# Performance work log

Measured on AMD Instinct MI355X. Metric: run time of the kernel, lower is better.

## Reference

```python
import jax, jax.numpy as jnp
import numpy as np

N = 200_000   # nodes
E = 6_400_000 # edges (avg degree 32)


def setup_inputs() -> dict:
    key = jax.random.key(0)
    k = jax.random.split(key, 6)
    x = jax.random.normal(k[0], (N, 2), dtype=jnp.float32)
    edge_index = jax.random.randint(k[1], (2, E), 0, N, dtype=jnp.int32)
    # GCNConv(2, 8) and GCNConv(8, 4) parameters (Glorot-ish init, zero bias as in PyG)
    W1 = jax.random.normal(k[2], (2, 8), dtype=jnp.float32) * (1.0 / np.sqrt(2.0))
    b1 = jnp.zeros((8,), dtype=jnp.float32)
    W2 = jax.random.normal(k[3], (8, 4), dtype=jnp.float32) * (1.0 / np.sqrt(8.0))
    b2 = jnp.zeros((4,), dtype=jnp.float32)
    return {"x": x, "edge_index": edge_index, "W1": W1, "b1": b1, "W2": W2, "b2": b2}


def _gcn_conv(x, src, dst, norm, W, b, n):
    # PyG GCNConv: linear transform, normalized gather/scatter-add, bias after aggregation
    h = x @ W                                   # [N, F_out]
    msg = h[src] * norm[:, None]                # gather + edge-wise scale, [E', F_out]
    agg = jax.ops.segment_sum(msg, dst, num_segments=n)  # scatter-add at targets
    return agg + b


def reference(x, edge_index, W1, b1, W2, b2):
    n = x.shape[0]
    # add self-loops (PyG default add_self_loops=True)
    loops = jnp.arange(n, dtype=edge_index.dtype)
    src = jnp.concatenate([edge_index[0], loops])
    dst = jnp.concatenate([edge_index[1], loops])
    # symmetric degree normalization: deg computed at targets with unit edge weights
    deg = jax.ops.segment_sum(jnp.ones_like(src, dtype=x.dtype), dst, num_segments=n)
    deg_inv_sqrt = jnp.where(deg > 0, jax.lax.rsqrt(jnp.maximum(deg, 1.0)), 0.0)
    norm = deg_inv_sqrt[src] * deg_inv_sqrt[dst]  # [E']

    h = jax.nn.relu(_gcn_conv(x, src, dst, norm, W1, b1, n))
    out = _gcn_conv(h, src, dst, norm, W2, b2, n)
    return out
```

## Files before the change

kernel.cpp:

```cpp
#include <hip/hip_runtime.h>


#define EPB   8192
#define PART  2048
#define LPBIT 11
#define SRCB  18
#define BC    4
#define RSTR  2049
#define STCAP 17408
#define NB    128


__global__ __launch_bounds__(512) void countA_kernel(
    const int* __restrict__ dst, int* __restrict__ cntmat, int E, int P) {
    __shared__ int cnt[128];
    int tid = threadIdx.x;
    if (tid < 128) cnt[tid] = 0;
    __syncthreads();
    int nv4 = E >> 2;
    int b4 = (blockIdx.x * EPB) >> 2;
    int e4 = min(b4 + (EPB >> 2), nv4);
    const int4* d4 = (const int4*)dst;
    #pragma unroll
    for (int k = 0; k < (EPB >> 2); k += 512) {
        int i = b4 + k + tid;
        if (i < e4) {
            int4 d = d4[i];
            atomicAdd(&cnt[d.x >> LPBIT], 1);
            atomicAdd(&cnt[d.y >> LPBIT], 1);
            atomicAdd(&cnt[d.z >> LPBIT], 1);
            atomicAdd(&cnt[d.w >> LPBIT], 1);
        }
    }
    if (blockIdx.x == gridDim.x - 1) {
        int e = (nv4 << 2) + tid;
        if (e < E) atomicAdd(&cnt[dst[e] >> LPBIT], 1);
    }
    __syncthreads();
    int* row = cntmat + (size_t)blockIdx.x * P;
    if (tid < P) row[tid] = cnt[tid];
}

__global__ __launch_bounds__(256) void colscanA_kernel(
    int* __restrict__ cntmat, int* __restrict__ colTotal, int B, int P) {
    __shared__ int sdata[256];
    int p = blockIdx.x, tid = threadIdx.x;
    int v[4];
    int s = 0;
    #pragma unroll
    for (int k = 0; k < 4; k++) {
        int b = tid * 4 + k;
        v[k] = (b < B) ? cntmat[(size_t)b * P + p] : 0;
        s += v[k];
    }
    int x = s;
    sdata[tid] = x;
    __syncthreads();
    for (int off = 1; off < 256; off <<= 1) {
        int t = (tid >= off) ? sdata[tid - off] : 0;
        __syncthreads();
        x += t;
        sdata[tid] = x;
        __syncthreads();
    }
    int run = x - s;
    #pragma unroll
    for (int k = 0; k < 4; k++) {
        int b = tid * 4 + k;
        if (b < B) cntmat[(size_t)b * P + p] = run;
        run += v[k];
    }
    if (tid == 255) colTotal[p] = x;
}

__global__ __launch_bounds__(256) void totalscanA_kernel(
    const int* __restrict__ colTotal, int* __restrict__ colStart,
    int P, int E) {
    __shared__ int sdata[256];
    int tid = threadIdx.x;
    int v[4];
    int s = 0;
    #pragma unroll
    for (int k = 0; k < 4; k++) {
        int i = tid * 4 + k;
        v[k] = (i < P) ? colTotal[i] : 0;
        s += v[k];
    }
    int x = s;
    sdata[tid] = x;
    __syncthreads();
    for (int off = 1; off < 256; off <<= 1) {
        int t = (tid >= off) ? sdata[tid - off] : 0;
        __syncthreads();
        x += t;
        sdata[tid] = x;
        __syncthreads();
    }
    int run = x - s;
    #pragma unroll
    for (int k = 0; k < 4; k++) {
        int i = tid * 4 + k;
        if (i < P) colStart[i] = run;
        run += v[k];
    }
    if (tid == 0) colStart[P] = E;
}

__global__ __launch_bounds__(512) void scatterA_kernel(
    const int* __restrict__ src, const int* __restrict__ dst,
    const int* __restrict__ cntmat, const int* __restrict__ colStart,
    unsigned* __restrict__ packed, int E, int P) {
    __shared__ int cur[128];
    int tid = threadIdx.x;
    if (tid < P) cur[tid] = colStart[tid] + cntmat[(size_t)blockIdx.x * P + tid];
    __syncthreads();
    int nv4 = E >> 2;
    int b4 = (blockIdx.x * EPB) >> 2;
    int e4 = min(b4 + (EPB >> 2), nv4);
    const int4* d4 = (const int4*)dst;
    const int4* s4 = (const int4*)src;
    #pragma unroll
    for (int k = 0; k < (EPB >> 2); k += 512) {
        int i = b4 + k + tid;
        if (i < e4) {
            int4 d = d4[i];
            int4 sv = s4[i];
            int p0 = atomicAdd(&cur[d.x >> LPBIT], 1);
            packed[p0] = ((unsigned)(d.x & (PART - 1)) << SRCB) | (unsigned)sv.x;
            int p1 = atomicAdd(&cur[d.y >> LPBIT], 1);
            packed[p1] = ((unsigned)(d.y & (PART - 1)) << SRCB) | (unsigned)sv.y;
            int p2 = atomicAdd(&cur[d.z >> LPBIT], 1);
            packed[p2] = ((unsigned)(d.z & (PART - 1)) << SRCB) | (unsigned)sv.z;
            int p3 = atomicAdd(&cur[d.w >> LPBIT], 1);
            packed[p3] = ((unsigned)(d.w & (PART - 1)) << SRCB) | (unsigned)sv.w;
        }
    }
    if (blockIdx.x == gridDim.x - 1) {
        int e = (nv4 << 2) + tid;
        if (e < E) {
            int d = dst[e];
            int pos = atomicAdd(&cur[d >> LPBIT], 1);
            packed[pos] = ((unsigned)(d & (PART - 1)) << SRCB) | (unsigned)src[e];
        }
    }
}


__global__ __launch_bounds__(512) void localC_kernel(
    const unsigned* __restrict__ packed, const int* __restrict__ colStart,
    int* __restrict__ runStart, int* __restrict__ sorted) {
    __shared__ int hist[PART];
    __shared__ int sdata[512];
    __shared__ unsigned stage[STCAP];
    int tid = threadIdx.x;
    int dp = blockIdx.x >> 2, b = blockIdx.x & (BC - 1);
    int s0 = colStart[dp], len = colStart[dp + 1] - s0;
    int lo = s0 + (int)(((long long)len * b) / BC);
    int hi = s0 + (int)(((long long)len * (b + 1)) / BC);
    for (int k = tid; k < PART; k += 512) hist[k] = 0;
    __syncthreads();
    for (int i = lo + tid; i < hi; i += 512)
        atomicAdd(&hist[packed[i] >> SRCB], 1);
    __syncthreads();
    int off = tid * 4;
    int v0 = hist[off], v1 = hist[off + 1], v2 = hist[off + 2], v3 = hist[off + 3];
    int s = v0 + v1 + v2 + v3;
    int x = s;
    sdata[tid] = x;
    __syncthreads();
    for (int o = 1; o < 512; o <<= 1) {
        int t = (tid >= o) ? sdata[tid - o] : 0;
        __syncthreads();
        x += t;
        sdata[tid] = x;
        __syncthreads();
    }
    int run = x - s;
    int* rs = runStart + (size_t)(dp * BC + b) * RSTR;
    int c0 = lo + run, c1 = c0 + v0, c2 = c1 + v1, c3 = c2 + v2;
    rs[off] = c0; rs[off + 1] = c1; rs[off + 2] = c2; rs[off + 3] = c3;
    __syncthreads();
    hist[off] = c0; hist[off + 1] = c1; hist[off + 2] = c2; hist[off + 3] = c3;
    if (tid == 0) rs[PART] = hi;
    __syncthreads();
    int total = hi - lo;
    bool ovf = total > STCAP;
    for (int i = lo + tid; i < hi; i += 512) {
        unsigned w = packed[i];
        int pos = atomicAdd(&hist[w >> SRCB], 1);
        if (!ovf) stage[pos - lo] = w;
        else sorted[pos] = (int)w;
    }
    __syncthreads();
    if (!ovf)
        for (int j = tid; j < total; j += 512) sorted[lo + j] = (int)stage[j];
}


__global__ __launch_bounds__(512) void dinvg_kernel(
    const int* __restrict__ runStart, const float* __restrict__ x,
    float* __restrict__ dinv, float* __restrict__ g, int n) {
    int i = blockIdx.x * 512 + threadIdx.x;
    if (i >= n) return;
    int dp = i >> LPBIT, ld = i & (PART - 1);
    int deg = 0;
    #pragma unroll
    for (int b = 0; b < BC; b++) {
        const int* rs = runStart + (size_t)(dp * BC + b) * RSTR + ld;
        deg += rs[1] - rs[0];
    }
    float d = rsqrtf((float)deg + 1.0f);
    dinv[i] = d;
    float2 xv = ((const float2*)x)[i];
    ((float2*)g)[i] = make_float2(xv.x * d, xv.y * d);
}


__global__ __launch_bounds__(512) void agg1f_kernel(
    const int* __restrict__ sorted, const int* __restrict__ runStart,
    const float* __restrict__ g, const float* __restrict__ dinv,
    const float* __restrict__ W1, const float* __restrict__ b1,
    const float* __restrict__ W2, float* __restrict__ hs2, int n) {
    __shared__ float acc[NB * 2];
    int tid = threadIdx.x;
    int i0 = blockIdx.x * NB;
    int dp = i0 >> LPBIT, l0 = i0 & (PART - 1);
    for (int k = tid; k < NB * 2; k += 512) acc[k] = 0.0f;
    __syncthreads();
    int lane = tid & 63;
    #pragma unroll
    for (int b = 0; b < BC; b++) {
        const int* rs = runStart + (size_t)(dp * BC + b) * RSTR;
        int lo = rs[l0], hi = rs[l0 + NB];
        for (int base = lo; base < hi; base += 512) {
            int e = base + tid;
            int sid = -1;
            float s0 = 0.0f, s1 = 0.0f;
            if (e < hi) {
                unsigned w = (unsigned)sorted[e];
                sid = (int)(w >> SRCB) - l0;
                int src = (int)(w & ((1u << SRCB) - 1));
                float2 gv = ((const float2*)g)[src];
                s0 = gv.x; s1 = gv.y;
            }
            #pragma unroll
            for (int off = 1; off < 64; off <<= 1) {
                int ps = __shfl_up(sid, off);
                float p0 = __shfl_up(s0, off);
                float p1 = __shfl_up(s1, off);
                if (lane >= off && ps == sid) { s0 += p0; s1 += p1; }
            }
            int ns = __shfl_down(sid, 1);
            bool tail = (lane == 63) || (ns != sid);
            if (tail && sid >= 0) {
                atomicAdd(&acc[sid * 2],     s0);
                atomicAdd(&acc[sid * 2 + 1], s1);
            }
        }
    }
    __syncthreads();
    if (tid < NB) {
        int i = i0 + tid;
        if (i < n) {
            float d = dinv[i];
            float2 gi = ((const float2*)g)[i];
            float s0 = (acc[tid * 2]     + gi.x) * d;
            float s1 = (acc[tid * 2 + 1] + gi.y) * d;
            float oc0 = 0.0f, oc1 = 0.0f, oc2 = 0.0f, oc3 = 0.0f;
            #pragma unroll
            for (int f = 0; f < 8; f++) {
                float h = fmaxf(s0 * W1[f] + s1 * W1[8 + f] + b1[f], 0.0f);
                oc0 += h * W2[4 * f];
                oc1 += h * W2[4 * f + 1];
                oc2 += h * W2[4 * f + 2];
                oc3 += h * W2[4 * f + 3];
            }
            float4 o;
            o.x = oc0 * d; o.y = oc1 * d; o.z = oc2 * d; o.w = oc3 * d;
            ((float4*)hs2)[i] = o;
        }
    }
}

__global__ __launch_bounds__(512) void agg2f_kernel(
    const int* __restrict__ sorted, const int* __restrict__ runStart,
    const float* __restrict__ hs2, const float* __restrict__ dinv,
    const float* __restrict__ b2, float* __restrict__ out, int n) {
    __shared__ float acc[NB * 4];
    int tid = threadIdx.x;
    int i0 = blockIdx.x * NB;
    int dp = i0 >> LPBIT, l0 = i0 & (PART - 1);
    for (int k = tid; k < NB * 4; k += 512) acc[k] = 0.0f;
    __syncthreads();
    int lane = tid & 63;
    #pragma unroll
    for (int b = 0; b < BC; b++) {
        const int* rs = runStart + (size_t)(dp * BC + b) * RSTR;
        int lo = rs[l0], hi = rs[l0 + NB];
        for (int base = lo; base < hi; base += 512) {
            int e = base + tid;
            int sid = -1;
            float s0 = 0.0f, s1 = 0.0f, s2 = 0.0f, s3 = 0.0f;
            if (e < hi) {
                unsigned w = (unsigned)sorted[e];
                sid = (int)(w >> SRCB) - l0;
                int src = (int)(w & ((1u << SRCB) - 1));
                float4 hv = ((const float4*)hs2)[src];
                s0 = hv.x; s1 = hv.y; s2 = hv.z; s3 = hv.w;
            }
            #pragma unroll
            for (int off = 1; off < 64; off <<= 1) {
                int ps = __shfl_up(sid, off);
                float p0 = __shfl_up(s0, off);
                float p1 = __shfl_up(s1, off);
                float p2 = __shfl_up(s2, off);
                float p3 = __shfl_up(s3, off);
                if (lane >= off && ps == sid) { s0 += p0; s1 += p1; s2 += p2; s3 += p3; }
            }
            int ns = __shfl_down(sid, 1);
            bool tail = (lane == 63) || (ns != sid);
            if (tail && sid >= 0) {
                atomicAdd(&acc[sid * 4],     s0);
                atomicAdd(&acc[sid * 4 + 1], s1);
                atomicAdd(&acc[sid * 4 + 2], s2);
                atomicAdd(&acc[sid * 4 + 3], s3);
            }
        }
    }
    __syncthreads();
    if (tid < NB) {
        int i = i0 + tid;
        if (i < n) {
            float d = dinv[i];
            float4 hv = ((const float4*)hs2)[i];
            float4 o;
            o.x = d * (acc[tid * 4]     + hv.x) + b2[0];
            o.y = d * (acc[tid * 4 + 1] + hv.y) + b2[1];
            o.z = d * (acc[tid * 4 + 2] + hv.z) + b2[2];
            o.w = d * (acc[tid * 4 + 3] + hv.w) + b2[3];
            ((float4*)out)[i] = o;
        }
    }
}

extern "C" void kernel_launch(void* const* d_in, const int* in_sizes, int n_in,
                              void* d_out, int out_size, void* d_ws, size_t ws_size,
                              hipStream_t stream) {
    const float* x   = (const float*)d_in[0];
    const int*   ei  = (const int*)d_in[1];
    const float* W1  = (const float*)d_in[2];
    const float* b1  = (const float*)d_in[3];
    const float* W2  = (const float*)d_in[4];
    const float* b2  = (const float*)d_in[5];
    float* out = (float*)d_out;

    const int n = in_sizes[0] / 2;
    const int E = in_sizes[1] / 2;
    const int* src = ei;
    const int* dst = ei + E;

    const int P  = (n + PART - 1) >> LPBIT;
    const int B1 = (E + EPB - 1) / EPB;

    int* ws = (int*)d_ws;
    int* colTotal = ws;
    int* colStart = ws + 1024;
    int* cntmatA  = ws + 2048;
    size_t cmsz = (((size_t)B1 * P) + 3) & ~(size_t)3;
    int* runStart = cntmatA + cmsz;
    size_t rssz = (((size_t)P * BC * RSTR) + 3) & ~(size_t)3;
    unsigned* packed = (unsigned*)(runStart + rssz);
    int* sorted = (int*)(packed + E);
    size_t nd = (size_t)P << LPBIT;
    float* dinv = (float*)packed;
    float* g    = dinv + nd;
    float* hs2  = g + 2 * nd;

    const int gN = (n + 511) / 512;
    const int gB = (n + NB - 1) / NB;

    countA_kernel    <<<B1, 512, 0, stream>>>(dst, cntmatA, E, P);
    colscanA_kernel  <<<P, 256, 0, stream>>>(cntmatA, colTotal, B1, P);
    totalscanA_kernel<<<1, 256, 0, stream>>>(colTotal, colStart, P, E);
    scatterA_kernel  <<<B1, 512, 0, stream>>>(src, dst, cntmatA, colStart, packed, E, P);
    localC_kernel    <<<P * BC, 512, 0, stream>>>(packed, colStart, runStart, sorted);
    dinvg_kernel     <<<gN, 512, 0, stream>>>(runStart, x, dinv, g, n);
    agg1f_kernel     <<<gB, 512, 0, stream>>>(sorted, runStart, g, dinv, W1, b1, W2, hs2, n);
    agg2f_kernel     <<<gB, 512, 0, stream>>>(sorted, runStart, hs2, dinv, b2, out, n);
}
```

Baseline: 272.1 us.

## Replace segmented wave-scan aggregation with LDS-staged gather and per-node reduction

```diff
diff --git a/kernel.cpp b/kernel.cpp
--- a/kernel.cpp
+++ b/kernel.cpp
@@ -9,6 +9,7 @@
 #define RSTR  2049
 #define STCAP 17408
 #define NB    128
+#define CAP   1536
 
 
 __global__ __launch_bounds__(512) void countA_kernel(
@@ -216,56 +217,61 @@
 }
 
 
-__global__ __launch_bounds__(512) void agg1f_kernel(
+__global__ __launch_bounds__(512) void agg1s_kernel(
     const int* __restrict__ sorted, const int* __restrict__ runStart,
     const float* __restrict__ g, const float* __restrict__ dinv,
     const float* __restrict__ W1, const float* __restrict__ b1,
     const float* __restrict__ W2, float* __restrict__ hs2, int n) {
-    __shared__ float acc[NB * 2];
+    __shared__ float2 stage2[CAP];
+    __shared__ int sb[BC][NB + 1];
+    __shared__ float sres[NB * 2];
+    float* stage = (float*)stage2;
     int tid = threadIdx.x;
     int i0 = blockIdx.x * NB;
     int dp = i0 >> LPBIT, l0 = i0 & (PART - 1);
-    for (int k = tid; k < NB * 2; k += 512) acc[k] = 0.0f;
-    __syncthreads();
-    int lane = tid & 63;
+    for (int k = tid; k < BC * (NB + 1); k += 512) {
+        int b = k / (NB + 1), idx = k - b * (NB + 1);
+        sb[b][idx] = runStart[(size_t)(dp * BC + b) * RSTR + l0 + idx];
+    }
+    int nid = tid >> 2;
+    int c = tid & 1;
+    int half = (tid >> 1) & 1;
+    float acc = 0.0f;
+    __syncthreads();
     #pragma unroll
     for (int b = 0; b < BC; b++) {
-        const int* rs = runStart + (size_t)(dp * BC + b) * RSTR;
-        int lo = rs[l0], hi = rs[l0 + NB];
-        for (int base = lo; base < hi; base += 512) {
-            int e = base + tid;
-            int sid = -1;
-            float s0 = 0.0f, s1 = 0.0f;
-            if (e < hi) {
+        int lo = sb[b][0], hi = sb[b][NB];
+        for (int e = lo + tid; e < hi; e += 512) {
+            int off = e - lo;
+            if (off < CAP) {
                 unsigned w = (unsigned)sorted[e];
-                sid = (int)(w >> SRCB) - l0;
                 int src = (int)(w & ((1u << SRCB) - 1));
-                float2 gv = ((const float2*)g)[src];
-                s0 = gv.x; s1 = gv.y;
-            }
-            #pragma unroll
-            for (int off = 1; off < 64; off <<= 1) {
-                int ps = __shfl_up(sid, off);
-                float p0 = __shfl_up(s0, off);
-                float p1 = __shfl_up(s1, off);
-                if (lane >= off && ps == sid) { s0 += p0; s1 += p1; }
-            }
-            int ns = __shfl_down(sid, 1);
-            bool tail = (lane == 63) || (ns != sid);
-            if (tail && sid >= 0) {
-                atomicAdd(&acc[sid * 2],     s0);
-                atomicAdd(&acc[sid * 2 + 1], s1);
-            }
-        }
-    }
+                stage2[off] = ((const float2*)g)[src];
+            }
+        }
+        __syncthreads();
+        int a = sb[b][nid] - lo, bnd = sb[b][nid + 1] - lo;
+        for (int j = a + half; j < bnd; j += 2) {
+            if (j < CAP) acc += stage[j * 2 + c];
+            else {
+                unsigned w = (unsigned)sorted[lo + j];
+                int src = (int)(w & ((1u << SRCB) - 1));
+                acc += g[2 * (size_t)src + c];
+            }
+        }
+        __syncthreads();
+    }
+    if (half == 1) sres[nid * 2 + c] = acc;
+    __syncthreads();
+    if (half == 0) sres[nid * 2 + c] += acc;
     __syncthreads();
     if (tid < NB) {
         int i = i0 + tid;
         if (i < n) {
             float d = dinv[i];
             float2 gi = ((const float2*)g)[i];
-            float s0 = (acc[tid * 2]     + gi.x) * d;
-            float s1 = (acc[tid * 2 + 1] + gi.y) * d;
+            float s0 = (sres[tid * 2] + gi.x) * d;
+            float s1 = (sres[tid * 2 + 1] + gi.y) * d;
             float oc0 = 0.0f, oc1 = 0.0f, oc2 = 0.0f, oc3 = 0.0f;
             #pragma unroll
             for (int f = 0; f < 8; f++) {
@@ -282,64 +288,51 @@
     }
 }
 
-__global__ __launch_bounds__(512) void agg2f_kernel(
+__global__ __launch_bounds__(512) void agg2s_kernel(
     const int* __restrict__ sorted, const int* __restrict__ runStart,
     const float* __restrict__ hs2, const float* __restrict__ dinv,
     const float* __restrict__ b2, float* __restrict__ out, int n) {
-    __shared__ float acc[NB * 4];
+    __shared__ float4 stage4[CAP];
+    __shared__ int sb[BC][NB + 1];
+    float* stage = (float*)stage4;
     int tid = threadIdx.x;
     int i0 = blockIdx.x * NB;
     int dp = i0 >> LPBIT, l0 = i0 & (PART - 1);
-    for (int k = tid; k < NB * 4; k += 512) acc[k] = 0.0f;
-    __syncthreads();
-    int lane = tid & 63;
+    for (int k = tid; k < BC * (NB + 1); k += 512) {
+        int b = k / (NB + 1), idx = k - b * (NB + 1);
+        sb[b][idx] = runStart[(size_t)(dp * BC + b) * RSTR + l0 + idx];
+    }
+    int nid = tid >> 2, c = tid & 3;
+    float acc = 0.0f;
+    __syncthreads();
     #pragma unroll
     for (int b = 0; b < BC; b++) {
-        const int* rs = runStart + (size_t)(dp * BC + b) * RSTR;
-        int lo = rs[l0], hi = rs[l0 + NB];
-        for (int base = lo; base < hi; base += 512) {
-            int e = base + tid;
-            int sid = -1;
-            float s0 = 0.0f, s1 = 0.0f, s2 = 0.0f, s3 = 0.0f;
-            if (e < hi) {
+        int lo = sb[b][0], hi = sb[b][NB];
+        for (int e = lo + tid; e < hi; e += 512) {
+            int off = e - lo;
+            if (off < CAP) {
                 unsigned w = (unsigned)sorted[e];
-                sid = (int)(w >> SRCB) - l0;
                 int src = (int)(w & ((1u << SRCB) - 1));
-                float4 hv = ((const float4*)hs2)[src];
-                s0 = hv.x; s1 = hv.y; s2 = hv.z; s3 = hv.w;
-            }
-            #pragma unroll
-            for (int off = 1; off < 64; off <<= 1) {
-                int ps = __shfl_up(sid, off);
-                float p0 = __shfl_up(s0, off);
-                float p1 = __shfl_up(s1, off);
-                float p2 = __shfl_up(s2, off);
-                float p3 = __shfl_up(s3, off);
-                if (lane >= off && ps == sid) { s0 += p0; s1 += p1; s2 += p2; s3 += p3; }
-            }
-            int ns = __shfl_down(sid, 1);
-            bool tail = (lane == 63) || (ns != sid);
-            if (tail && sid >= 0) {
-                atomicAdd(&acc[sid * 4],     s0);
-                atomicAdd(&acc[sid * 4 + 1], s1);
-                atomicAdd(&acc[sid * 4 + 2], s2);
-                atomicAdd(&acc[sid * 4 + 3], s3);
-            }
-        }
-    }
-    __syncthreads();
-    if (tid < NB) {
-        int i = i0 + tid;
-        if (i < n) {
-            float d = dinv[i];
-            float4 hv = ((const float4*)hs2)[i];
-            float4 o;
-            o.x = d * (acc[tid * 4]     + hv.x) + b2[0];
-            o.y = d * (acc[tid * 4 + 1] + hv.y) + b2[1];
-            o.z = d * (acc[tid * 4 + 2] + hv.z) + b2[2];
-            o.w = d * (acc[tid * 4 + 3] + hv.w) + b2[3];
-            ((float4*)out)[i] = o;
-        }
+                stage4[off] = ((const float4*)hs2)[src];
+            }
+        }
+        __syncthreads();
+        int a = sb[b][nid] - lo, bnd = sb[b][nid + 1] - lo;
+        for (int j = a; j < bnd; j++) {
+            if (j < CAP) acc += stage[j * 4 + c];
+            else {
+                unsigned w = (unsigned)sorted[lo + j];
+                int src = (int)(w & ((1u << SRCB) - 1));
+                acc += hs2[4 * (size_t)src + c];
+            }
+        }
+        __syncthreads();
+    }
+    int i = i0 + nid;
+    if (i < n) {
+        float d = dinv[i];
+        float hv = hs2[4 * (size_t)i + c];
+        out[4 * (size_t)i + c] = d * (acc + hv) + b2[c];
     }
 }
 
@@ -385,6 +378,6 @@
     scatterA_kernel  <<<B1, 512, 0, stream>>>(src, dst, cntmatA, colStart, packed, E, P);
     localC_kernel    <<<P * BC, 512, 0, stream>>>(packed, colStart, runStart, sorted);
     dinvg_kernel     <<<gN, 512, 0, stream>>>(runStart, x, dinv, g, n);
-    agg1f_kernel     <<<gB, 512, 0, stream>>>(sorted, runStart, g, dinv, W1, b1, W2, hs2, n);
-    agg2f_kernel     <<<gB, 512, 0, stream>>>(sorted, runStart, hs2, dinv, b2, out, n);
-}
+    agg1s_kernel     <<<gB, 512, 0, stream>>>(sorted, runStart, g, dinv, W1, b1, W2, hs2, n);
+    agg2s_kernel     <<<gB, 512, 0, stream>>>(sorted, runStart, hs2, dinv, b2, out, n);
+}
```

Measured after the change: 245.2 us. 1.11x faster.
